# Kernel optimization log

Hardware: AMD Instinct MI355X
Metric: run time of the kernel (lower is better)

## Reference

```python
import jax, jax.numpy as jnp
import numpy as np

B, N = 32, 512            # batch, max nodes per graph
F_DIM, M_DIM = 1024, 256  # node feature dim, first hidden dim
N_SEM = 8                 # number of semantic-class experts
XYZ, DIM_E = 3, 8
OUT_SIZE = 2 * XYZ + DIM_E  # 14 (default reg branch)
EPS = 1e-8                # padding value used by out_seq_to_batch


def setup_inputs() -> dict:
    key = jax.random.key(0)
    ks = jax.random.split(key, 12)
    def w(k, shape, fan_in):
        return jax.random.normal(k, shape, jnp.float32) / np.float32(np.sqrt(fan_in))
    return {
        "nodes": jax.random.normal(ks[0], (B, N, F_DIM), jnp.float32),
        "sem": jax.random.randint(ks[1], (B, N), 0, N_SEM, jnp.int32),
        "lengths": jax.random.randint(ks[2], (B,), 64, N + 1, jnp.int32),
        # y expert MLPs (4 layers), stacked over experts
        "W1": w(ks[3], (N_SEM, F_DIM, M_DIM), F_DIM), "b1": jnp.zeros((N_SEM, M_DIM), jnp.float32),
        "W2": w(ks[4], (N_SEM, M_DIM, 64), M_DIM),   "b2": jnp.zeros((N_SEM, 64), jnp.float32),
        "W3": w(ks[5], (N_SEM, 64, 32), 64),         "b3": jnp.zeros((N_SEM, 32), jnp.float32),
        "W4": w(ks[6], (N_SEM, 32, OUT_SIZE), 32),   "b4": jnp.zeros((N_SEM, OUT_SIZE), jnp.float32),
        # rot expert MLPs (2 layers), stacked over experts
        "R1": w(ks[7], (N_SEM, F_DIM, M_DIM), F_DIM), "rb1": jnp.zeros((N_SEM, M_DIM), jnp.float32),
        "R2": w(ks[8], (N_SEM, M_DIM, XYZ), M_DIM),   "rb2": jnp.zeros((N_SEM, XYZ), jnp.float32),
    }


def _prim_mlps(nodes, sem, lengths, W1, b1, W2, b2, W3, b3, W4, b4, R1, rb1, R2, rb2):
    Bn, Nn, Fd = nodes.shape
    x = nodes.reshape(-1, Fd)                       # [T, F], T = B*N tokens
    semf = sem.reshape(-1)                          # [T] expert id per token
    # dense dispatch: run every expert on all tokens, then select per token
    h1 = jax.nn.relu(jnp.einsum('tf,efm->etm', x, W1) + b1[:, None, :])   # [E,T,M]
    h2 = jax.nn.relu(jnp.einsum('etm,emh->eth', h1, W2) + b2[:, None, :]) # [E,T,64]
    h3 = jax.nn.relu(jnp.einsum('eth,ehg->etg', h2, W3) + b3[:, None, :]) # [E,T,32]
    y_all = jnp.einsum('etg,ego->eto', h3, W4) + b4[:, None, :]           # [E,T,OUT]
    r1 = jax.nn.relu(jnp.einsum('tf,efm->etm', x, R1) + rb1[:, None, :])  # [E,T,M]
    rot_all = jnp.einsum('etm,emo->eto', r1, R2) + rb2[:, None, :]        # [E,T,XYZ]
    t = jnp.arange(x.shape[0])
    y = y_all[semf, t]                              # [T, OUT]
    rot = rot_all[semf, t]                          # [T, XYZ]
    out = jnp.concatenate([y, rot], axis=-1).reshape(Bn, Nn, -1)
    # positions beyond each graph's length are filled with eps (out_seq_to_batch)
    mask = (jnp.arange(Nn)[None, :] < lengths[:, None])[:, :, None]
    return jnp.where(mask, out, jnp.float32(EPS))


def reference(nodes, sem, lengths, W1, b1, W2, b2, W3, b3, W4, b4, R1, rb1, R2, rb2):
    return _prim_mlps(nodes, sem, lengths, W1, b1, W2, b2, W3, b3, W4, b4,
                      R1, rb1, R2, rb2)
```

## Files before the change

### kernel.cpp

```cpp
#include <hip/hip_runtime.h>
#include <stdint.h>

#define T_TOK 16384
#define NE 8
#define EPSV 1e-8f
#define MAXC64  264
#define MAXC16  1032

#define WS_PERM   0
#define WS_PART   65536
#define WS_OFFS   67584
#define WS_WT     131072
#define WS_H1     (WS_WT + 8*512*1024*2)
#define WS_W2T    (WS_H1 + 16448*512*2)
#define WS_W3T    (WS_W2T + 8*64*256*2)
#define WS_W4T    (WS_W3T + 8*32*64*2)
#define WS_R2T    (WS_W4T + 8*16*32*2)

typedef __attribute__((ext_vector_type(8))) short bf16x8;
typedef __attribute__((ext_vector_type(4))) float f32x4;

__device__ __forceinline__ unsigned short f2bf(float f) {
    unsigned u = __float_as_uint(f);
    u += 0x7fffu + ((u >> 16) & 1u);
    return (unsigned short)(u >> 16);
}

__device__ __forceinline__ void cvt_wr16(short* dst, float4 a, float4 b) {
    unsigned u0 = (unsigned)f2bf(a.x) | ((unsigned)f2bf(a.y) << 16);
    unsigned u1 = (unsigned)f2bf(a.z) | ((unsigned)f2bf(a.w) << 16);
    unsigned u2 = (unsigned)f2bf(b.x) | ((unsigned)f2bf(b.y) << 16);
    unsigned u3 = (unsigned)f2bf(b.z) | ((unsigned)f2bf(b.w) << 16);
    *(uint4*)dst = make_uint4(u0, u1, u2, u3);
}

__device__ __forceinline__ void gl_lds16(const void* g, void* l) {
    __builtin_amdgcn_global_load_lds(
        (const __attribute__((address_space(1))) void*)g,
        (__attribute__((address_space(3))) void*)l,
        16, 0, 0);
}

__device__ __forceinline__ bool chunk_lookup(const int* __restrict__ offs, int c, int csize,
                                             int& e, int& base, int& len) {
    int acc = 0;
#pragma unroll
    for (int i = 0; i < NE; i++) {
        int s = offs[i], t = offs[i + 1];
        int cc = (t - s + csize - 1) / csize;
        if (c < acc + cc) {
            e = i;
            base = s + (c - acc) * csize;
            len = (t - base < csize) ? (t - base) : csize;
            return true;
        }
        acc += cc;
    }
    return false;
}

__global__ __launch_bounds__(256) void k_prep1(const float* __restrict__ W1,
                                               const float* __restrict__ R1,
                                               const float* __restrict__ W2,
                                               const float* __restrict__ W3,
                                               const float* __restrict__ W4,
                                               const float* __restrict__ R2,
                                               const int* __restrict__ sem,
                                               unsigned short* __restrict__ wt,
                                               unsigned short* __restrict__ w2t,
                                               unsigned short* __restrict__ w3t,
                                               unsigned short* __restrict__ w4t,
                                               unsigned short* __restrict__ r2t,
                                               int* __restrict__ ws_i) {
    __shared__ float tile[64][65];
    int id = blockIdx.x, tid = threadIdx.x;
    if (id >= 1024) {
        __shared__ int cnt[NE];
        int hb = id - 1024, lane = tid & 63;
        if (tid < NE) cnt[tid] = 0;
        __syncthreads();
        int s = sem[hb * 256 + tid];
#pragma unroll
        for (int e = 0; e < NE; e++) {
            unsigned long long m = __ballot(s == e);
            if (lane == e) atomicAdd(&cnt[e], (int)__popcll(m));
        }
        __syncthreads();
        if (tid < NE) ws_i[(WS_PART >> 2) + hb * NE + tid] = cnt[tid];
        return;
    }
    int e = id >> 7, rem = id & 127;
    int ny = rem >> 4, kx = rem & 15;
    int k0 = kx * 64, n0 = ny * 64;
    const float* src = (n0 < 256) ? (W1 + (size_t)e * 1024 * 256 + n0)
                                  : (R1 + (size_t)e * 1024 * 256 + (n0 - 256));
    int rr = tid >> 4;
    int cg = (tid & 15) * 4;
#pragma unroll
    for (int p = 0; p < 4; p++) {
        int kk = p * 16 + rr;
        float4 v = *(const float4*)(src + (size_t)(k0 + kk) * 256 + cg);
        tile[kk][cg] = v.x; tile[kk][cg + 1] = v.y; tile[kk][cg + 2] = v.z; tile[kk][cg + 3] = v.w;
    }
    __syncthreads();
    int nn = tid >> 3;
    int k8 = tid & 7;
#pragma unroll
    for (int p = 0; p < 2; p++) {
        int n = p * 32 + nn;
        unsigned w[4];
#pragma unroll
        for (int j = 0; j < 4; j++) {
            float f0 = tile[k8 * 8 + 2 * j][n];
            float f1 = tile[k8 * 8 + 2 * j + 1][n];
            w[j] = (unsigned)f2bf(f0) | ((unsigned)f2bf(f1) << 16);
        }
        *(uint4*)(wt + (size_t)(e * 512 + n0 + n) * 1024 + k0 + k8 * 8) =
            make_uint4(w[0], w[1], w[2], w[3]);
    }
    if (ny == 0) {
        int x = kx;
        for (int j = tid; j < 1024; j += 256) {
            int idx = x * 1024 + j; int k = idx & 255, n = idx >> 8;
            w2t[(size_t)(e * 64 + n) * 256 + k] = f2bf(W2[(size_t)e * 16384 + k * 64 + n]);
        }
        if (tid < 128) {
            int idx = x * 128 + tid; int k = idx & 63, n = idx >> 6;
            w3t[(size_t)(e * 32 + n) * 64 + k] = f2bf(W3[(size_t)e * 2048 + k * 32 + n]);
        }
        if (tid < 32) {
            int idx = x * 32 + tid; int k = idx & 31, n = idx >> 5;
            w4t[(size_t)(e * 16 + n) * 32 + k] = (n < 14) ? f2bf(W4[(size_t)e * 448 + k * 14 + n])
                                                          : (unsigned short)0;
        }
        {
            int idx = x * 256 + tid; int k = idx & 255, n = idx >> 8;
            r2t[(size_t)(e * 16 + n) * 256 + k] = (n < 3) ? f2bf(R2[(size_t)e * 768 + k * 3 + n])
                                                          : (unsigned short)0;
        }
    }
}

__global__ __launch_bounds__(256) void k_perm(const int* __restrict__ sem,
                                              int* __restrict__ ws_i) {
    __shared__ int parts[512];
    __shared__ int tot[NE], preb[NE], ebase[NE + 1];
    __shared__ int wcnt[4][NE];
    int g = blockIdx.x;
    int tid = threadIdx.x, wave = tid >> 6, lane = tid & 63;
    parts[tid] = ws_i[(WS_PART >> 2) + tid];
    parts[256 + tid] = ws_i[(WS_PART >> 2) + 256 + tid];
    __syncthreads();
    if (tid < NE) {
        int t = 0, p = 0;
        for (int bb = 0; bb < 64; bb++) {
            int v = parts[bb * NE + tid];
            t += v;
            if (bb < g) p += v;
        }
        tot[tid] = t; preb[tid] = p;
    }
    __syncthreads();
    if (tid == 0) {
        int base = 0;
        for (int e = 0; e < NE; e++) { ebase[e] = base; base += tot[e]; }
        ebase[NE] = base;
        if (g == 0)
            for (int e = 0; e <= NE; e++) ws_i[(WS_OFFS >> 2) + e] = ebase[e];
    }
    int i = g * 256 + tid;
    int s = sem[i];
    int rank = 0;
#pragma unroll
    for (int e = 0; e < NE; e++) {
        unsigned long long m = __ballot(s == e);
        if (s == e) rank = (int)__popcll(m & ((1ull << lane) - 1ull));
        if (lane == e) wcnt[wave][e] = (int)__popcll(m);
    }
    __syncthreads();
    int wpre = 0;
#pragma unroll
    for (int w = 0; w < 4; w++)
        if (w < wave) wpre += wcnt[w][s];
    int dest = ebase[s] + preb[s] + wpre + rank;
    ws_i[(WS_PERM >> 2) + dest] = i;
}

__global__ __launch_bounds__(256) void k_gemm(const float* __restrict__ nodes,
                                              const unsigned short* __restrict__ wt,
                                              const float* __restrict__ b1,
                                              const float* __restrict__ rb1,
                                              const int* __restrict__ ws_i,
                                              unsigned short* __restrict__ h1) {
    __shared__ __align__(16) short As[2][64 * 64];
    __shared__ __align__(16) short Bs[2][128 * 64];
    int bid = blockIdx.x;
    int wgid = (bid & 7) * ((MAXC64 * 4) / 8) + (bid >> 3);
    int c = wgid >> 2, nblk = wgid & 3;
    int e, base, len;
    if (!chunk_lookup(ws_i + (WS_OFFS >> 2), c, 64, e, base, len)) return;
    int n0 = nblk * 128;
    int tid = threadIdx.x;
    int wave = tid >> 6, lane = tid & 63;
    int quad = lane >> 4, lr = lane & 15;
    int wn = wave * 32;

    f32x4 acc[4][2];
#pragma unroll
    for (int i = 0; i < 4; i++)
#pragma unroll
        for (int j = 0; j < 2; j++) acc[i][j] = (f32x4){0.f, 0.f, 0.f, 0.f};

    const int* perm = ws_i + (WS_PERM >> 2);
    const unsigned short* Bg = wt + (size_t)(e * 512 + n0) * 1024;

    const float* apA[2];
    int dstA[2];
#pragma unroll
    for (int i = 0; i < 2; i++) {
        int s = i * 256 + tid;
        int r = s >> 3, cs = (s & 7) ^ (r & 7);
        int gidx = base + r;
        if (gidx > T_TOK - 1) gidx = T_TOK - 1;
        int tok = perm[gidx];
        apA[i] = nodes + (size_t)tok * 1024 + cs * 8;
        dstA[i] = s * 8;
    }
    const unsigned short* srcB[4];
    int dstB[4];
#pragma unroll
    for (int i = 0; i < 4; i++) {
        int s = i * 256 + wave * 64 + lane;
        int r = s >> 3, cs = (s & 7) ^ (r & 7);
        srcB[i] = Bg + (size_t)r * 1024 + cs * 8;
        dstB[i] = (i * 256 + wave * 64) * 8;
    }

    float4 fa0, fb0, fa1, fb1;

    fa0 = *(const float4*)(apA[0]); fb0 = *(const float4*)(apA[0] + 4);
    fa1 = *(const float4*)(apA[1]); fb1 = *(const float4*)(apA[1] + 4);
#pragma unroll
    for (int i = 0; i < 4; i++) gl_lds16(srcB[i], &Bs[0][dstB[i]]);
    cvt_wr16(&As[0][dstA[0]], fa0, fb0);
    cvt_wr16(&As[0][dstA[1]], fa1, fb1);
    asm volatile("s_waitcnt vmcnt(0) lgkmcnt(0)" ::: "memory");
    __builtin_amdgcn_sched_barrier(0);
    __builtin_amdgcn_s_barrier();

    for (int kb = 0; kb < 16; kb++) {
        int cur = kb & 1;
        int nxt = cur ^ 1;
        if (kb < 15) {
            fa0 = *(const float4*)(apA[0] + (kb + 1) * 64);
            fb0 = *(const float4*)(apA[0] + (kb + 1) * 64 + 4);
            fa1 = *(const float4*)(apA[1] + (kb + 1) * 64);
            fb1 = *(const float4*)(apA[1] + (kb + 1) * 64 + 4);
#pragma unroll
            for (int i = 0; i < 4; i++) gl_lds16(srcB[i] + (kb + 1) * 64, &Bs[nxt][dstB[i]]);
        }
        __builtin_amdgcn_sched_barrier(0);

        const short* Ab = As[cur];
        const short* Bb = Bs[cur];
        bf16x8 af[2][4], bfr[2][2];
#pragma unroll
        for (int im = 0; im < 4; im++) {
            int r = im * 16 + lr;
#pragma unroll
            for (int kh = 0; kh < 2; kh++) {
                int q = kh * 4 + quad;
                af[kh][im] = *(const bf16x8*)(Ab + (r * 8 + (q ^ (r & 7))) * 8);
            }
        }
#pragma unroll
        for (int in = 0; in < 2; in++) {
            int r = wn + in * 16 + lr;
#pragma unroll
            for (int kh = 0; kh < 2; kh++) {
                int q = kh * 4 + quad;
                bfr[kh][in] = *(const bf16x8*)(Bb + (r * 8 + (q ^ (r & 7))) * 8);
            }
        }
#pragma unroll
        for (int kh = 0; kh < 2; kh++)
#pragma unroll
            for (int im = 0; im < 4; im++)
#pragma unroll
                for (int in = 0; in < 2; in++)
                    acc[im][in] = __builtin_amdgcn_mfma_f32_16x16x32_bf16(af[kh][im], bfr[kh][in], acc[im][in], 0, 0, 0);

        if (kb < 15) {
            cvt_wr16(&As[nxt][dstA[0]], fa0, fb0);
            cvt_wr16(&As[nxt][dstA[1]], fa1, fb1);
            asm volatile("s_waitcnt vmcnt(0) lgkmcnt(0)" ::: "memory");
            __builtin_amdgcn_sched_barrier(0);
            __builtin_amdgcn_s_barrier();
        }
    }

#pragma unroll
    for (int in = 0; in < 2; in++) {
        int gcol = n0 + wn + in * 16 + lr;
        float bias = (gcol < 256) ? b1[e * 256 + gcol] : rb1[e * 256 + gcol - 256];
#pragma unroll
        for (int im = 0; im < 4; im++) {
#pragma unroll
            for (int v = 0; v < 4; v++) {
                int r = im * 16 + quad * 4 + v;
                if (r < len) {
                    float val = fmaxf(acc[im][in][v] + bias, 0.f);
                    h1[(size_t)(base + r) * 512 + gcol] = f2bf(val);
                }
            }
        }
    }
}

__global__ __launch_bounds__(256) void k_tail(const unsigned short* __restrict__ h1,
                                              const int* __restrict__ ws_i,
                                              const unsigned short* __restrict__ w2t,
                                              const unsigned short* __restrict__ w3t,
                                              const unsigned short* __restrict__ w4t,
                                              const unsigned short* __restrict__ r2t,
                                              const float* __restrict__ b2,
                                              const float* __restrict__ b3,
                                              const float* __restrict__ b4,
                                              const float* __restrict__ rb2,
                                              const int* __restrict__ lengths,
                                              float* __restrict__ out) {
    __shared__ __align__(16) unsigned short h2s[16][64];
    __shared__ __align__(16) unsigned short h3s[16][32];

    int e, base, len;
    if (!chunk_lookup(ws_i + (WS_OFFS >> 2), blockIdx.x, 16, e, base, len)) return;
    int tid = threadIdx.x, wave = tid >> 6, lane = tid & 63;
    int quad = lane >> 4, lr = lane & 15;
    int lead = blockIdx.x & 3;

    const unsigned short* Ap = h1 + (size_t)base * 512;

    f32x4 acc2;
    { float bb = b2[e * 64 + wave * 16 + lr]; acc2 = (f32x4){bb, bb, bb, bb}; }
    f32x4 accr;
    { float bb = (lr < 3) ? rb2[e * 3 + lr] : 0.f; accr = (f32x4){bb, bb, bb, bb}; }

    const unsigned short* W2e = w2t + (size_t)e * 64 * 256;
    const unsigned short* R2e = r2t + (size_t)e * 16 * 256;
#pragma unroll
    for (int kk = 0; kk < 8; kk++) {
        int k0 = kk * 32;
        bf16x8 a = *(const bf16x8*)(Ap + lr * 512 + k0 + quad * 8);
        bf16x8 b = *(const bf16x8*)(W2e + (wave * 16 + lr) * 256 + k0 + quad * 8);
        acc2 = __builtin_amdgcn_mfma_f32_16x16x32_bf16(a, b, acc2, 0, 0, 0);
        if (wave == lead) {
            bf16x8 ar = *(const bf16x8*)(Ap + lr * 512 + 256 + k0 + quad * 8);
            bf16x8 br = *(const bf16x8*)(R2e + lr * 256 + k0 + quad * 8);
            accr = __builtin_amdgcn_mfma_f32_16x16x32_bf16(ar, br, accr, 0, 0, 0);
        }
    }
#pragma unroll
    for (int v = 0; v < 4; v++)
        h2s[quad * 4 + v][wave * 16 + lr] = f2bf(fmaxf(acc2[v], 0.f));
    __syncthreads();
    if (wave != lead) return;

    f32x4 acc3[2];
#pragma unroll
    for (int t = 0; t < 2; t++) {
        float bb = b3[e * 32 + t * 16 + lr];
        acc3[t] = (f32x4){bb, bb, bb, bb};
    }
    const unsigned short* W3e = w3t + (size_t)e * 32 * 64;
#pragma unroll
    for (int kk = 0; kk < 2; kk++) {
        int k0 = kk * 32;
        bf16x8 a = *(const bf16x8*)(&h2s[lr][k0 + quad * 8]);
#pragma unroll
        for (int t = 0; t < 2; t++) {
            bf16x8 b = *(const bf16x8*)(W3e + (t * 16 + lr) * 64 + k0 + quad * 8);
            acc3[t] = __builtin_amdgcn_mfma_f32_16x16x32_bf16(a, b, acc3[t], 0, 0, 0);
        }
    }
#pragma unroll
    for (int t = 0; t < 2; t++)
#pragma unroll
        for (int v = 0; v < 4; v++)
            h3s[quad * 4 + v][t * 16 + lr] = f2bf(fmaxf(acc3[t][v], 0.f));

    f32x4 acc4;
    { float bb = (lr < 14) ? b4[e * 14 + lr] : 0.f; acc4 = (f32x4){bb, bb, bb, bb}; }
    {
        bf16x8 a = *(const bf16x8*)(&h3s[lr][quad * 8]);
        bf16x8 b = *(const bf16x8*)(w4t + ((size_t)e * 16 + lr) * 32 + quad * 8);
        acc4 = __builtin_amdgcn_mfma_f32_16x16x32_bf16(a, b, acc4, 0, 0, 0);
    }

    const int* perm = ws_i + (WS_PERM >> 2);
#pragma unroll
    for (int v = 0; v < 4; v++) {
        int t = quad * 4 + v;
        if (t < len) {
            int token = perm[base + t];
            int bi = token >> 9, ni = token & 511;
            int valid = ni < lengths[bi];
            if (lr < 14) out[(size_t)token * 17 + lr] = valid ? acc4[v] : EPSV;
            if (lr < 3)  out[(size_t)token * 17 + 14 + lr] = valid ? accr[v] : EPSV;
        }
    }
}

extern "C" void kernel_launch(void* const* d_in, const int* in_sizes, int n_in,
                              void* d_out, int out_size, void* d_ws, size_t ws_size,
                              hipStream_t stream) {
    (void)in_sizes; (void)n_in; (void)out_size; (void)ws_size;
    const float* nodes   = (const float*)d_in[0];
    const int*   sem     = (const int*)d_in[1];
    const int*   lengths = (const int*)d_in[2];
    const float* W1 = (const float*)d_in[3];
    const float* b1 = (const float*)d_in[4];
    const float* W2 = (const float*)d_in[5];
    const float* b2 = (const float*)d_in[6];
    const float* W3 = (const float*)d_in[7];
    const float* b3 = (const float*)d_in[8];
    const float* W4 = (const float*)d_in[9];
    const float* b4 = (const float*)d_in[10];
    const float* R1  = (const float*)d_in[11];
    const float* rb1 = (const float*)d_in[12];
    const float* R2  = (const float*)d_in[13];
    const float* rb2 = (const float*)d_in[14];
    float* out = (float*)d_out;

    char* ws = (char*)d_ws;
    int* ws_i = (int*)ws;
    unsigned short* wt  = (unsigned short*)(ws + WS_WT);
    unsigned short* h1  = (unsigned short*)(ws + WS_H1);
    unsigned short* w2t = (unsigned short*)(ws + WS_W2T);
    unsigned short* w3t = (unsigned short*)(ws + WS_W3T);
    unsigned short* w4t = (unsigned short*)(ws + WS_W4T);
    unsigned short* r2t = (unsigned short*)(ws + WS_R2T);

    hipLaunchKernelGGL(k_prep1, dim3(1088), dim3(256), 0, stream,
                       W1, R1, W2, W3, W4, R2, sem, wt, w2t, w3t, w4t, r2t, ws_i);
    hipLaunchKernelGGL(k_perm, dim3(64), dim3(256), 0, stream, sem, ws_i);
    hipLaunchKernelGGL(k_gemm, dim3(MAXC64 * 4), dim3(256), 0, stream,
                       nodes, (const unsigned short*)wt, b1, rb1, (const int*)ws_i, h1);
    hipLaunchKernelGGL(k_tail, dim3(MAXC16), dim3(256), 0, stream,
                       (const unsigned short*)h1, (const int*)ws_i,
                       (const unsigned short*)w2t, (const unsigned short*)w3t,
                       (const unsigned short*)w4t, (const unsigned short*)r2t,
                       b2, b3, b4, rb2, lengths, out);
}
```

Before: 205.5 us.

## Prefetch A tiles two k-steps ahead with partial vmcnt waits in expert GEMM

Restructures the first-layer GEMM main loop into a manually unrolled pair of stages with separate even/odd register sets for the fp32 A tiles. The A loads for step kb+2 are issued before the barrier, and the wait becomes vmcnt(4), so those global loads can stay in flight across the next compute phase instead of fully draining every iteration. This is meant to hide global-load latency on the gathered node rows. The cost is more live registers, which could reduce occupancy, and the more delicate wait-count logic depends on the order in which loads are issued.

```diff
diff --git a/kernel.cpp b/kernel.cpp
--- a/kernel.cpp
+++ b/kernel.cpp
@@ -186,6 +186,46 @@
     ws_i[(WS_PERM >> 2) + dest] = i;
 }
 
+#define LOADA_E(kb) do { \
+    e0a = *(const float4*)(apA[0] + (kb) * 64); e0b = *(const float4*)(apA[0] + (kb) * 64 + 4); \
+    e1a = *(const float4*)(apA[1] + (kb) * 64); e1b = *(const float4*)(apA[1] + (kb) * 64 + 4); } while (0)
+#define LOADA_O(kb) do { \
+    o0a = *(const float4*)(apA[0] + (kb) * 64); o0b = *(const float4*)(apA[0] + (kb) * 64 + 4); \
+    o1a = *(const float4*)(apA[1] + (kb) * 64); o1b = *(const float4*)(apA[1] + (kb) * 64 + 4); } while (0)
+#define ISSUEB(kb, bufi) do { \
+    _Pragma("unroll") \
+    for (int i_ = 0; i_ < 4; i_++) gl_lds16(srcB[i_] + (kb) * 64, &Bs[bufi][dstB[i_]]); } while (0)
+#define COMPUTE(bufi) do { \
+    const short* Ab_ = As[bufi]; \
+    const short* Bb_ = Bs[bufi]; \
+    bf16x8 af_[2][4], bfr_[2][2]; \
+    _Pragma("unroll") \
+    for (int im_ = 0; im_ < 4; im_++) { \
+        int r_ = im_ * 16 + lr; \
+        _Pragma("unroll") \
+        for (int kh_ = 0; kh_ < 2; kh_++) { \
+            int q_ = kh_ * 4 + quad; \
+            af_[kh_][im_] = *(const bf16x8*)(Ab_ + (r_ * 8 + (q_ ^ (r_ & 7))) * 8); \
+        } \
+    } \
+    _Pragma("unroll") \
+    for (int in_ = 0; in_ < 2; in_++) { \
+        int r_ = wn + in_ * 16 + lr; \
+        _Pragma("unroll") \
+        for (int kh_ = 0; kh_ < 2; kh_++) { \
+            int q_ = kh_ * 4 + quad; \
+            bfr_[kh_][in_] = *(const bf16x8*)(Bb_ + (r_ * 8 + (q_ ^ (r_ & 7))) * 8); \
+        } \
+    } \
+    _Pragma("unroll") \
+    for (int kh_ = 0; kh_ < 2; kh_++) \
+    _Pragma("unroll") \
+    for (int im_ = 0; im_ < 4; im_++) \
+    _Pragma("unroll") \
+    for (int in_ = 0; in_ < 2; in_++) \
+        acc[im_][in_] = __builtin_amdgcn_mfma_f32_16x16x32_bf16(af_[kh_][im_], bfr_[kh_][in_], acc[im_][in_], 0, 0, 0); \
+    } while (0)
+
 __global__ __launch_bounds__(256) void k_gemm(const float* __restrict__ nodes,
                                               const unsigned short* __restrict__ wt,
                                               const float* __restrict__ b1,
@@ -236,68 +276,49 @@
         dstB[i] = (i * 256 + wave * 64) * 8;
     }
 
-    float4 fa0, fb0, fa1, fb1;
-
-    fa0 = *(const float4*)(apA[0]); fb0 = *(const float4*)(apA[0] + 4);
-    fa1 = *(const float4*)(apA[1]); fb1 = *(const float4*)(apA[1] + 4);
-#pragma unroll
-    for (int i = 0; i < 4; i++) gl_lds16(srcB[i], &Bs[0][dstB[i]]);
-    cvt_wr16(&As[0][dstA[0]], fa0, fb0);
-    cvt_wr16(&As[0][dstA[1]], fa1, fb1);
+    float4 e0a, e0b, e1a, e1b;
+    float4 o0a, o0b, o1a, o1b;
+
+    LOADA_E(0);
+    ISSUEB(0, 0);
+    __builtin_amdgcn_sched_barrier(0);
+    cvt_wr16(&As[0][dstA[0]], e0a, e0b);
+    cvt_wr16(&As[0][dstA[1]], e1a, e1b);
+    LOADA_O(1);
+    asm volatile("s_waitcnt vmcnt(4) lgkmcnt(0)" ::: "memory");
+    __builtin_amdgcn_sched_barrier(0);
+    __builtin_amdgcn_s_barrier();
+
+    for (int kb = 0; kb < 14; kb += 2) {
+        ISSUEB(kb + 1, 1);
+        __builtin_amdgcn_sched_barrier(0);
+        COMPUTE(0);
+        cvt_wr16(&As[1][dstA[0]], o0a, o0b);
+        cvt_wr16(&As[1][dstA[1]], o1a, o1b);
+        LOADA_E(kb + 2);
+        asm volatile("s_waitcnt vmcnt(4) lgkmcnt(0)" ::: "memory");
+        __builtin_amdgcn_sched_barrier(0);
+        __builtin_amdgcn_s_barrier();
+
+        ISSUEB(kb + 2, 0);
+        __builtin_amdgcn_sched_barrier(0);
+        COMPUTE(1);
+        cvt_wr16(&As[0][dstA[0]], e0a, e0b);
+        cvt_wr16(&As[0][dstA[1]], e1a, e1b);
+        LOADA_O(kb + 3);
+        asm volatile("s_waitcnt vmcnt(4) lgkmcnt(0)" ::: "memory");
+        __builtin_amdgcn_sched_barrier(0);
+        __builtin_amdgcn_s_barrier();
+    }
+    ISSUEB(15, 1);
+    __builtin_amdgcn_sched_barrier(0);
+    COMPUTE(0);
+    cvt_wr16(&As[1][dstA[0]], o0a, o0b);
+    cvt_wr16(&As[1][dstA[1]], o1a, o1b);
     asm volatile("s_waitcnt vmcnt(0) lgkmcnt(0)" ::: "memory");
     __builtin_amdgcn_sched_barrier(0);
     __builtin_amdgcn_s_barrier();
-
-    for (int kb = 0; kb < 16; kb++) {
-        int cur = kb & 1;
-        int nxt = cur ^ 1;
-        if (kb < 15) {
-            fa0 = *(const float4*)(apA[0] + (kb + 1) * 64);
-            fb0 = *(const float4*)(apA[0] + (kb + 1) * 64 + 4);
-            fa1 = *(const float4*)(apA[1] + (kb + 1) * 64);
-            fb1 = *(const float4*)(apA[1] + (kb + 1) * 64 + 4);
-#pragma unroll
-            for (int i = 0; i < 4; i++) gl_lds16(srcB[i] + (kb + 1) * 64, &Bs[nxt][dstB[i]]);
-        }
-        __builtin_amdgcn_sched_barrier(0);
-
-        const short* Ab = As[cur];
-        const short* Bb = Bs[cur];
-        bf16x8 af[2][4], bfr[2][2];
-#pragma unroll
-        for (int im = 0; im < 4; im++) {
-            int r = im * 16 + lr;
-#pragma unroll
-            for (int kh = 0; kh < 2; kh++) {
-                int q = kh * 4 + quad;
-                af[kh][im] = *(const bf16x8*)(Ab + (r * 8 + (q ^ (r & 7))) * 8);
-            }
-        }
-#pragma unroll
-        for (int in = 0; in < 2; in++) {
-            int r = wn + in * 16 + lr;
-#pragma unroll
-            for (int kh = 0; kh < 2; kh++) {
-                int q = kh * 4 + quad;
-                bfr[kh][in] = *(const bf16x8*)(Bb + (r * 8 + (q ^ (r & 7))) * 8);
-            }
-        }
-#pragma unroll
-        for (int kh = 0; kh < 2; kh++)
-#pragma unroll
-            for (int im = 0; im < 4; im++)
-#pragma unroll
-                for (int in = 0; in < 2; in++)
-                    acc[im][in] = __builtin_amdgcn_mfma_f32_16x16x32_bf16(af[kh][im], bfr[kh][in], acc[im][in], 0, 0, 0);
-
-        if (kb < 15) {
-            cvt_wr16(&As[nxt][dstA[0]], fa0, fb0);
-            cvt_wr16(&As[nxt][dstA[1]], fa1, fb1);
-            asm volatile("s_waitcnt vmcnt(0) lgkmcnt(0)" ::: "memory");
-            __builtin_amdgcn_sched_barrier(0);
-            __builtin_amdgcn_s_barrier();
-        }
-    }
+    COMPUTE(1);
 
 #pragma unroll
     for (int in = 0; in < 2; in++) {
```

After: 198.8 us. -3.3%, faster.
